# Performance work log

Hardware: AMD Instinct MI355X
Metric: run time of the kernel (lower is better)

## Reference

```python
import jax, jax.numpy as jnp
import numpy as np

B, NCROPS, T = 512, 5, 8192
NEG = -1e30  # masked fill for invalid (beyond-seqlen) positions


def setup_inputs() -> dict:
    key = jax.random.key(0)
    k1, k2, k3 = jax.random.split(key, 3)
    scores = jax.random.normal(k1, (B * NCROPS, T), dtype=jnp.float32)
    label = jax.random.randint(k2, (B,), 0, 2, dtype=jnp.int32)
    # valid lengths in [16, T] so that k = seqlen//16 + 1 is always in range
    seqlen = jax.random.randint(k3, (B,), 16, T + 1, dtype=jnp.int32)
    return {"scores": scores, "label": label, "seqlen": seqlen}


def reference(scores, label, seqlen):
    # uncrop 'mean': [B*ncrops, T] -> [B, T]
    s = scores.reshape(B, NCROPS, T).mean(axis=1)

    # mask invalid positions, sort each row descending (vectorized ragged top-k)
    valid = jnp.arange(T)[None, :] < seqlen[:, None]            # [B, T]
    s_sorted = -jnp.sort(-jnp.where(valid, s, NEG), axis=1)     # descending
    csum = jnp.cumsum(s_sorted, axis=1)                         # [B, T]

    # get_k: label==0 -> 1; k==-1 -> seqlen//16 + 1 (k-1 < seqlen always)
    k = jnp.where(label == 0, 1, seqlen // 16 + 1)              # [B]
    topk_sum = jnp.take_along_axis(csum, (k - 1)[:, None], axis=1)[:, 0]
    vl_scores = topk_sum / k.astype(s.dtype)                    # mean of top-k

    # BCEWithLogitsLoss (mean reduction): logaddexp(0, v) - v*y
    y = label.astype(s.dtype)
    loss = jnp.mean(jnp.logaddexp(0.0, vl_scores) - vl_scores * y)
    return loss
```

## Files before the change

kernel.cpp:

```cpp
#include <hip/hip_runtime.h>
#include <stdint.h>

#define BB      512
#define NCROPS  5
#define TT      8192
#define THREADS 512
#define WAVES   8

__device__ __forceinline__ uint32_t f2ord(float f) {
    uint32_t b = __float_as_uint(f);
    return (b & 0x80000000u) ? ~b : (b | 0x80000000u);
}
__device__ __forceinline__ float ord2f(uint32_t u) {
    uint32_t b = (u & 0x80000000u) ? (u & 0x7FFFFFFFu) : ~u;
    return __uint_as_float(b);
}

#define FOR4(OP) OP(u0) OP(u1) OP(u2) OP(u3)

__global__ __launch_bounds__(THREADS, 4) void topk_loss_rows(
    const float* __restrict__ scores, const int* __restrict__ label,
    const int* __restrict__ seqlen, float* __restrict__ row_loss)
{
    const int b    = blockIdx.x;
    const int tid  = threadIdx.x;
    const int lane = tid & 63;
    const int wave = tid >> 6;

    const int sl = seqlen[b];
    const int lb = label[b];
    const int k  = (lb == 0) ? 1 : (sl / 16 + 1);

    __shared__ uint32_t hist[2][WAVES][256];
    __shared__ uint32_t bc_p, bc_k;
    __shared__ uint32_t s_m[WAVES];
    __shared__ float    s_s[WAVES];
    __shared__ int      s_c[WAVES];

    const float* base = scores + (size_t)b * NCROPS * TT;
    #define LOADJ(A0,A1,A2,A3,A4, J, PRED) \
        const bool PRED = (4 * (tid + (J) * THREADS) < sl); \
        float4 A0, A1, A2, A3, A4; \
        if (PRED) { \
            const int t4 = tid + (J) * THREADS; \
            A0 = *reinterpret_cast<const float4*>(base + 0 * TT + 4 * t4); \
            A1 = *reinterpret_cast<const float4*>(base + 1 * TT + 4 * t4); \
            A2 = *reinterpret_cast<const float4*>(base + 2 * TT + 4 * t4); \
            A3 = *reinterpret_cast<const float4*>(base + 3 * TT + 4 * t4); \
            A4 = *reinterpret_cast<const float4*>(base + 4 * TT + 4 * t4); \
        }
    LOADJ(a0,b0,c0,d0,e0, 0, p0)
    LOADJ(a1,b1,c1,d1,e1, 1, p1)
    LOADJ(a2,b2,c2,d2,e2, 2, p2)
    LOADJ(a3,b3,c3,d3,e3, 3, p3)

    {
        uint32_t* hz = &hist[0][0][0];
        #pragma unroll
        for (int i = 0; i < 4; ++i) hz[tid + i * THREADS] = 0u;
    }
    __syncthreads();

    uint4 u0, u1, u2, u3;
    #define KEYJ(DST, A0,A1,A2,A3,A4, J, PRED) \
        if (PRED) { \
            const int t0 = 4 * (tid + (J) * THREADS); \
            float4 a; \
            a.x = (A0.x + A1.x + A2.x + A3.x + A4.x) * 0.2f; \
            a.y = (A0.y + A1.y + A2.y + A3.y + A4.y) * 0.2f; \
            a.z = (A0.z + A1.z + A2.z + A3.z + A4.z) * 0.2f; \
            a.w = (A0.w + A1.w + A2.w + A3.w + A4.w) * 0.2f; \
            DST.x = f2ord(a.x); \
            DST.y = (t0 + 1 < sl) ? f2ord(a.y) : 0u; \
            DST.z = (t0 + 2 < sl) ? f2ord(a.z) : 0u; \
            DST.w = (t0 + 3 < sl) ? f2ord(a.w) : 0u; \
        } else { \
            DST.x = 0u; DST.y = 0u; DST.z = 0u; DST.w = 0u; \
        }
    KEYJ(u0, a0,b0,c0,d0,e0, 0, p0)
    KEYJ(u1, a1,b1,c1,d1,e1, 1, p1)
    KEYJ(u2, a2,b2,c2,d2,e2, 2, p2)
    KEYJ(u3, a3,b3,c3,d3,e3, 3, p3)

    uint32_t thr;
    if (k == 1) {
        uint32_t mx = 0u;
        #define MAXOP(V) mx = max(mx, max(max(V.x, V.y), max(V.z, V.w)));
        FOR4(MAXOP)
        #pragma unroll
        for (int off = 32; off; off >>= 1) {
            const uint32_t o = (uint32_t)__shfl_down((int)mx, off);
            mx = max(mx, o);
        }
        if (lane == 0) s_m[wave] = mx;
        __syncthreads();
        uint32_t rowmax = s_m[0];
        #pragma unroll
        for (int w = 1; w < WAVES; ++w) rowmax = max(rowmax, s_m[w]);
        thr = rowmax;
    } else {
        uint32_t p = 0u, kr = (uint32_t)k;
        #pragma unroll
        for (int r = 0; r < 4; ++r) {
            uint32_t* h = &hist[r & 1][wave][0];
            if (r == 0) {
                #define H0(X)  if ((X) != 0u) atomicAdd(&h[(X) >> 24], 1u);
                #define H0V(V) H0(V.x) H0(V.y) H0(V.z) H0(V.w)
                FOR4(H0V)
            } else {
                const int shp = 32 - 8 * r;
                const int shd = shp - 8;
                #define HR(X)  if ((X) != 0u && ((X) >> shp) == p) atomicAdd(&h[((X) >> shd) & 255u], 1u);
                #define HRV(V) HR(V.x) HR(V.y) HR(V.z) HR(V.w)
                FOR4(HRV)
            }
            __syncthreads();
            if (wave == 0) {
                uint32_t t0s = 0u, t1s = 0u, t2s = 0u, t3s = 0u;
                #pragma unroll
                for (int w = 0; w < WAVES; ++w) {
                    const uint32_t* hw = &hist[r & 1][w][0];
                    t0s += hw[4 * lane + 0];
                    t1s += hw[4 * lane + 1];
                    t2s += hw[4 * lane + 2];
                    t3s += hw[4 * lane + 3];
                }
                const uint32_t s = t0s + t1s + t2s + t3s;
                uint32_t suf = s;
                #pragma unroll
                for (int off = 1; off < 64; off <<= 1) {
                    const uint32_t v = (uint32_t)__shfl_down((int)suf, off);
                    if (lane + off < 64) suf += v;
                }
                const uint32_t E  = suf - s;
                const uint32_t T3 = E  + t3s;
                const uint32_t T2 = T3 + t2s;
                const uint32_t T1 = T2 + t1s;
                const uint32_t T0 = T1 + t0s;
                const unsigned long long bal = __ballot(T0 >= kr);
                const int L = 63 - __clzll(bal);
                if (lane == L) {
                    uint32_t j, Tj, tj;
                    if      (T3 >= kr) { j = 3u; Tj = T3; tj = t3s; }
                    else if (T2 >= kr) { j = 2u; Tj = T2; tj = t2s; }
                    else if (T1 >= kr) { j = 1u; Tj = T1; tj = t1s; }
                    else               { j = 0u; Tj = T0; tj = t0s; }
                    bc_p = (p << 8) | (uint32_t)(4 * lane) | j;
                    bc_k = kr - (Tj - tj);
                }
            } else if (r < 3) {
                uint32_t* hz = &hist[(r + 1) & 1][0][0];
                for (int i = tid - 64; i < 2048; i += (THREADS - 64)) hz[i] = 0u;
            }
            __syncthreads();
            p  = bc_p;
            kr = bc_k;
        }
        thr = p;
    }

    float sg = 0.f;
    int   cg = 0;
    #define SUMOP(V) \
        if (V.x >= thr) { sg += ord2f(V.x); cg++; } \
        if (V.y >= thr) { sg += ord2f(V.y); cg++; } \
        if (V.z >= thr) { sg += ord2f(V.z); cg++; } \
        if (V.w >= thr) { sg += ord2f(V.w); cg++; }
    FOR4(SUMOP)
    #pragma unroll
    for (int off = 32; off; off >>= 1) {
        sg += __shfl_down(sg, off);
        cg += __shfl_down(cg, off);
    }
    if (lane == 0) { s_s[wave] = sg; s_c[wave] = cg; }
    __syncthreads();

    if (tid == 0) {
        float S = 0.f; int C = 0;
        #pragma unroll
        for (int w = 0; w < WAVES; ++w) { S += s_s[w]; C += s_c[w]; }
        const float kf   = ord2f(thr);
        const float topk = S - (float)(C - k) * kf;
        const float v    = topk / (float)k;
        const float y    = (float)lb;
        const float la   = fmaxf(v, 0.f) + log1pf(expf(-fabsf(v)));
        row_loss[b] = la - v * y;
    }
}

__global__ __launch_bounds__(256) void reduce_loss(
    const float* __restrict__ row_loss, float* __restrict__ out)
{
    const int tid = threadIdx.x;
    float v = row_loss[tid] + row_loss[tid + 256];
    #pragma unroll
    for (int off = 32; off; off >>= 1) v += __shfl_down(v, off);
    __shared__ float s[4];
    if ((tid & 63) == 0) s[tid >> 6] = v;
    __syncthreads();
    if (tid == 0) out[0] = (s[0] + s[1] + s[2] + s[3]) * (1.0f / 512.0f);
}

extern "C" void kernel_launch(void* const* d_in, const int* in_sizes, int n_in,
                              void* d_out, int out_size, void* d_ws, size_t ws_size,
                              hipStream_t stream) {
    const float* scores = (const float*)d_in[0];
    const int*   label  = (const int*)d_in[1];
    const int*   seqlen = (const int*)d_in[2];
    float* out      = (float*)d_out;
    float* row_loss = (float*)d_ws;

    topk_loss_rows<<<BB, THREADS, 0, stream>>>(scores, label, seqlen, row_loss);
    reduce_loss<<<1, 256, 0, stream>>>(row_loss, out);
}
```

Before: 22.12 us.

## Schedule rows by length for load balance, pad histograms, fuse final reduction

Adds a one-block scheduling kernel that counting-sorts rows by sequence length and interleaves long and short rows, so that the blocks processing heavy rows are dispatched first and co-scheduled with light ones. The main kernel reads its row index from this order. Histogram rows are padded to 257 entries to reduce LDS bank conflicts. The separate reduction kernel is replaced by a last-block-done atomic pattern, at the cost of an added memset and an extra small scheduling launch.

```diff
diff --git a/kernel.cpp b/kernel.cpp
--- a/kernel.cpp
+++ b/kernel.cpp
@@ -6,6 +6,7 @@
 #define TT      8192
 #define THREADS 512
 #define WAVES   8
+#define HPAD    257
 
 __device__ __forceinline__ uint32_t f2ord(float f) {
     uint32_t b = __float_as_uint(f);
@@ -16,28 +17,69 @@
     return __uint_as_float(b);
 }
 
-#define FOR4(OP) OP(u0) OP(u1) OP(u2) OP(u3)
-
-__global__ __launch_bounds__(THREADS, 4) void topk_loss_rows(
-    const float* __restrict__ scores, const int* __restrict__ label,
-    const int* __restrict__ seqlen, float* __restrict__ row_loss)
+__global__ __launch_bounds__(512) void schedule_rows(
+    const int* __restrict__ seqlen, int* __restrict__ order)
 {
-    const int b    = blockIdx.x;
     const int tid  = threadIdx.x;
     const int lane = tid & 63;
     const int wave = tid >> 6;
-
-    const int sl = seqlen[b];
-    const int lb = label[b];
+    __shared__ uint32_t cnt[512];
+    __shared__ uint32_t wsum[8];
+
+    cnt[tid] = 0u;
+    __syncthreads();
+
+    const int sl = seqlen[tid];
+    const uint32_t bucket = (uint32_t)(8192 - sl) >> 4;
+    const uint32_t pos = atomicAdd(&cnt[bucket], 1u);
+    __syncthreads();
+
+    const uint32_t v = cnt[tid];
+    int inc = (int)v;
+    #pragma unroll
+    for (int off = 1; off < 64; off <<= 1) {
+        const int t = __shfl_up(inc, off);
+        if (lane >= off) inc += t;
+    }
+    if (lane == 63) wsum[wave] = (uint32_t)inc;
+    __syncthreads();
+    uint32_t woff = 0u;
+    for (int w = 0; w < wave; ++w) woff += wsum[w];
+    const uint32_t excl = woff + (uint32_t)inc - v;
+    __syncthreads();
+    cnt[tid] = excl;
+    __syncthreads();
+
+    const uint32_t rank = cnt[bucket] + pos;
+    const uint32_t slot = (rank < 256u) ? rank : (767u - rank);
+    order[slot] = tid;
+}
+
+#define FOR4(OP) OP(u0) OP(u1) OP(u2) OP(u3)
+
+__global__ __launch_bounds__(THREADS, 4) void topk_loss_rows(
+    const float* __restrict__ scores, const int* __restrict__ label,
+    const int* __restrict__ seqlen, const int* __restrict__ order,
+    float* __restrict__ row_loss, uint32_t* __restrict__ done,
+    float* __restrict__ out)
+{
+    const int tid  = threadIdx.x;
+    const int lane = tid & 63;
+    const int wave = tid >> 6;
+    const int row  = order[blockIdx.x];
+
+    const int sl = seqlen[row];
+    const int lb = label[row];
     const int k  = (lb == 0) ? 1 : (sl / 16 + 1);
 
-    __shared__ uint32_t hist[2][WAVES][256];
+    __shared__ uint32_t hist[2][WAVES][HPAD];
     __shared__ uint32_t bc_p, bc_k;
     __shared__ uint32_t s_m[WAVES];
     __shared__ float    s_s[WAVES];
     __shared__ int      s_c[WAVES];
-
-    const float* base = scores + (size_t)b * NCROPS * TT;
+    __shared__ int      s_last;
+
+    const float* base = scores + (size_t)row * NCROPS * TT;
     #define LOADJ(A0,A1,A2,A3,A4, J, PRED) \
         const bool PRED = (4 * (tid + (J) * THREADS) < sl); \
         float4 A0, A1, A2, A3, A4; \
@@ -56,8 +98,7 @@
 
     {
         uint32_t* hz = &hist[0][0][0];
-        #pragma unroll
-        for (int i = 0; i < 4; ++i) hz[tid + i * THREADS] = 0u;
+        for (int i = tid; i < WAVES * HPAD; i += THREADS) hz[i] = 0u;
     }
     __syncthreads();
 
@@ -150,7 +191,7 @@
                 }
             } else if (r < 3) {
                 uint32_t* hz = &hist[(r + 1) & 1][0][0];
-                for (int i = tid - 64; i < 2048; i += (THREADS - 64)) hz[i] = 0u;
+                for (int i = tid - 64; i < WAVES * HPAD; i += (THREADS - 64)) hz[i] = 0u;
             }
             __syncthreads();
             p  = bc_p;
@@ -184,21 +225,26 @@
         const float v    = topk / (float)k;
         const float y    = (float)lb;
         const float la   = fmaxf(v, 0.f) + log1pf(expf(-fabsf(v)));
-        row_loss[b] = la - v * y;
-    }
-}
-
-__global__ __launch_bounds__(256) void reduce_loss(
-    const float* __restrict__ row_loss, float* __restrict__ out)
-{
-    const int tid = threadIdx.x;
-    float v = row_loss[tid] + row_loss[tid + 256];
-    #pragma unroll
-    for (int off = 32; off; off >>= 1) v += __shfl_down(v, off);
-    __shared__ float s[4];
-    if ((tid & 63) == 0) s[tid >> 6] = v;
-    __syncthreads();
-    if (tid == 0) out[0] = (s[0] + s[1] + s[2] + s[3]) * (1.0f / 512.0f);
+        row_loss[row] = la - v * y;
+        __threadfence();
+        s_last = (atomicAdd(done, 1u) == (uint32_t)(BB - 1));
+    }
+    __syncthreads();
+
+    if (s_last) {
+        __threadfence();
+        float v = row_loss[tid];
+        #pragma unroll
+        for (int off = 32; off; off >>= 1) v += __shfl_down(v, off);
+        if (lane == 0) s_s[wave] = v;
+        __syncthreads();
+        if (tid == 0) {
+            float S = 0.f;
+            #pragma unroll
+            for (int w = 0; w < WAVES; ++w) S += s_s[w];
+            out[0] = S * (1.0f / (float)BB);
+        }
+    }
 }
 
 extern "C" void kernel_launch(void* const* d_in, const int* in_sizes, int n_in,
@@ -207,9 +253,14 @@
     const float* scores = (const float*)d_in[0];
     const int*   label  = (const int*)d_in[1];
     const int*   seqlen = (const int*)d_in[2];
-    float* out      = (float*)d_out;
-    float* row_loss = (float*)d_ws;
-
-    topk_loss_rows<<<BB, THREADS, 0, stream>>>(scores, label, seqlen, row_loss);
-    reduce_loss<<<1, 256, 0, stream>>>(row_loss, out);
-}
+    float* out = (float*)d_out;
+
+    int*      order    = (int*)d_ws;
+    float*    row_loss = (float*)((char*)d_ws + 2048);
+    uint32_t* done     = (uint32_t*)((char*)d_ws + 4096);
+
+    hipMemsetAsync(done, 0, sizeof(uint32_t), stream);
+    schedule_rows<<<1, 512, 0, stream>>>(seqlen, order);
+    topk_loss_rows<<<BB, THREADS, 0, stream>>>(scores, label, seqlen, order,
+                                               row_loss, done, out);
+}
```

Result: slower. 32.47 us (+46.8%).
